# Kernel tuning notes

Measured on AMD Instinct MI355X. Metric: run time of the kernel, lower is better.

Reference implementation:

```python
import jax, jax.numpy as jnp
import numpy as np

N = 50000          # nodes
E = 1_600_000      # edges (avg degree 32)
IN_N, IN_E = 16, 1 # fc_encoder hardwired input dims
H = 128            # per-layer out_node/out_edge channels (out//2 = 64 inner)
BN_EPS = 1e-5


def setup_inputs() -> dict:
    key = jax.random.key(0)
    ks = jax.random.split(key, 32)
    d = {}
    d["x"] = jax.random.normal(ks[0], (N, IN_N), jnp.float32)
    d["edge_attr"] = jax.random.normal(ks[1], (E, IN_E), jnp.float32)
    d["edge_index"] = jax.random.randint(ks[2], (2, E), 0, N)
    i = 3
    for l, (ni, ei) in enumerate([(IN_N, IN_E), (H, H)]):
        s_n = 1.0 / np.sqrt(ni)
        s_e = 1.0 / np.sqrt(ei)
        s_h = 1.0 / np.sqrt(H)
        d[f"l{l}_Wn"] = jax.random.normal(ks[i], (H // 2, ni), jnp.float32) * s_n; i += 1
        d[f"l{l}_We"] = jax.random.normal(ks[i], (H // 2, ei), jnp.float32) * s_e; i += 1
        d[f"l{l}_Wfn"] = jax.random.normal(ks[i], (H, H), jnp.float32) * s_h; i += 1
        d[f"l{l}_bfn"] = jax.random.normal(ks[i], (H,), jnp.float32) * s_h; i += 1
        d[f"l{l}_Wfe"] = jax.random.normal(ks[i], (H, H), jnp.float32) * s_h; i += 1
        d[f"l{l}_bfe"] = jax.random.normal(ks[i], (H,), jnp.float32) * s_h; i += 1
        d[f"l{l}_g"] = jax.random.uniform(ks[i], (H,), jnp.float32, 0.5, 1.5); i += 1
        d[f"l{l}_b"] = jax.random.normal(ks[i], (H,), jnp.float32) * 0.1; i += 1
        d[f"l{l}_rm"] = jax.random.normal(ks[i], (H,), jnp.float32) * 0.1; i += 1
        d[f"l{l}_rv"] = jax.random.uniform(ks[i], (H,), jnp.float32, 0.5, 1.5); i += 1
    return d


def _layer(x, ea, src, dst, Wn, We, Wfn, bfn, Wfe, bfe, g, b, rm, rv):
    # NodeEdgeInteraction_node (eval mode: dropout = identity)
    n1 = jax.nn.relu(x @ Wn.T)            # [N, H/2]
    e1 = jax.nn.relu(ea @ We.T)           # [E, H/2]
    # edge_updater: cat([n1[src] + n1[dst], e1])
    e2 = jnp.concatenate([n1[src] + n1[dst], e1], axis=-1)      # [E, H]
    # propagate: message = e1, sum-aggregate at destination (edge_index[1])
    agg = jax.ops.segment_sum(e1, dst, num_segments=x.shape[0])  # [N, H/2]
    n2 = jnp.concatenate([agg, n1], axis=-1)                     # [N, H]
    n2 = jax.nn.relu(n2 @ Wfn.T + bfn)
    e2 = jax.nn.relu(e2 @ Wfe.T + bfe)
    # BatchNorm1d (eval: running stats)
    n2 = (n2 - rm) * jax.lax.rsqrt(rv + BN_EPS) * g + b
    return n2, e2


def reference(x, edge_attr, edge_index,
              l0_Wn, l0_We, l0_Wfn, l0_bfn, l0_Wfe, l0_bfe, l0_g, l0_b, l0_rm, l0_rv,
              l1_Wn, l1_We, l1_Wfn, l1_bfn, l1_Wfe, l1_bfe, l1_g, l1_b, l1_rm, l1_rv):
    src, dst = edge_index[0], edge_index[1]
    x, edge_attr = _layer(x, edge_attr, src, dst,
                          l0_Wn, l0_We, l0_Wfn, l0_bfn, l0_Wfe, l0_bfe,
                          l0_g, l0_b, l0_rm, l0_rv)
    x, edge_attr = _layer(x, edge_attr, src, dst,
                          l1_Wn, l1_We, l1_Wfn, l1_bfn, l1_Wfe, l1_bfe,
                          l1_g, l1_b, l1_rm, l1_rv)
    return x  # GNNEncoder returns node embeddings only
```

## Files before the change

kernel.cpp:

```cpp
#include <hip/hip_runtime.h>

typedef unsigned short u16;
typedef __attribute__((ext_vector_type(8))) short short8;
typedef __attribute__((ext_vector_type(4))) float floatx4;

#define NN 50000
#define NE 1600000
#define BN_EPS 1e-5f

__device__ __forceinline__ float bfu(u16 u) {
    union { unsigned u32; float f; } v; v.u32 = ((unsigned)u) << 16; return v.f;
}
__device__ __forceinline__ u16 f2bf(float f) {
    union { float f; unsigned u; } v; v.f = f;
    unsigned r = v.u + 0x7FFFu + ((v.u >> 16) & 1u);
    return (u16)(r >> 16);
}
__device__ __forceinline__ float ldf(const void* p, int i, int m) {
    return m ? ((const float*)p)[i] : bfu(((const u16*)p)[i]);
}

__global__ __launch_bounds__(256) void k_detect(const u16* __restrict__ x, int* __restrict__ mode) {
    float mx = 0.f;
    for (int i = threadIdx.x; i < 4096; i += 256) mx = fmaxf(mx, fabsf(bfu(x[i])));
#pragma unroll
    for (int o = 32; o > 0; o >>= 1) mx = fmaxf(mx, __shfl_down(mx, o));
    __shared__ float s[4];
    if ((threadIdx.x & 63) == 0) s[threadIdx.x >> 6] = mx;
    __syncthreads();
    if (threadIdx.x == 0) {
        float m2 = fmaxf(fmaxf(s[0], s[1]), fmaxf(s[2], s[3]));
        mode[0] = (m2 > 1e4f) ? 1 : 0;
    }
}

__global__ __launch_bounds__(256) void k_cvtw(const void* __restrict__ W0, const void* __restrict__ W1,
                                              const void* __restrict__ W2, const void* __restrict__ W3,
                                              const void* __restrict__ W4,
                                              u16* __restrict__ dst, const int* __restrict__ mf) {
    int m = mf[0];
    int i = blockIdx.x * 256 + threadIdx.x;
    const void* src; int off;
    if (i < 16384)      { src = W0; off = i; }
    else if (i < 24576) { src = W1; off = i - 16384; }
    else if (i < 40960) { src = W2; off = i - 24576; }
    else if (i < 49152) { src = W3; off = i - 40960; }
    else                { src = W4; off = i - 49152; }
    dst[i] = m ? f2bf(((const float*)src)[off]) : ((const u16*)src)[off];
}

__global__ __launch_bounds__(256) void k_enc0(const void* __restrict__ x, const void* __restrict__ Wn,
                                              u16* __restrict__ n1, const int* __restrict__ mf) {
    int m = mf[0];
    __shared__ float Wns[64 * 17];
    __shared__ float xsh[4][16];
    int t = threadIdx.x;
    int n0 = blockIdx.x * 4;
    for (int i = t; i < 1024; i += 256) Wns[(i >> 4) * 17 + (i & 15)] = ldf(Wn, i, m);
    if (t < 64) xsh[t >> 4][t & 15] = ldf(x, n0 * 16 + t, m);
    __syncthreads();
    int n = t >> 6, c = t & 63;
    float acc = 0.f;
#pragma unroll
    for (int i = 0; i < 16; i++) acc += xsh[n][i] * Wns[c * 17 + i];
    n1[(n0 + n) * 64 + c] = f2bf(fmaxf(acc, 0.f));
}

__global__ __launch_bounds__(256) void k_esum(const void* __restrict__ ea, const int* __restrict__ ei,
                                              float* __restrict__ sp, float* __restrict__ sn,
                                              const int* __restrict__ mf) {
    int m = mf[0];
    int e = blockIdx.x * 256 + threadIdx.x;
    float a = ldf(ea, e, m);
    int d = ei[NE + e];
    if (a > 0.f) atomicAdd(sp + d, a);
    else if (a < 0.f) atomicAdd(sn + d, a);
}

__global__ void k_pn(const void* __restrict__ We0, const void* __restrict__ Wfe0,
                     float* __restrict__ PN, const int* __restrict__ mf) {
    int m = mf[0];
    int j = threadIdx.x;
    float p = 0.f, n = 0.f;
    for (int k = 0; k < 64; k++) {
        float w = ldf(We0, k, m);
        float wf = ldf(Wfe0, j * 128 + 64 + k, m);
        p += fmaxf(w, 0.f) * wf;
        n += fminf(w, 0.f) * wf;
    }
    PN[j] = p; PN[128 + j] = n;
}

__global__ __launch_bounds__(256) void k_node_l0(
    const u16* __restrict__ n1l0, const float* __restrict__ sp, const float* __restrict__ sn,
    const void* __restrict__ We0, const u16* __restrict__ Wfn0c, const void* __restrict__ bfn0,
    const void* __restrict__ g0, const void* __restrict__ b0,
    const void* __restrict__ rm0, const void* __restrict__ rv0,
    const u16* __restrict__ Wn1c, u16* __restrict__ n1l1, const int* __restrict__ mf) {
    int m = mf[0];
    __shared__ __align__(16) u16 fs[64][136];
    __shared__ __align__(16) u16 xs[64][136];
    int t = threadIdx.x;
    int n0 = blockIdx.x * 64;
    {
        int col = t & 127;
        int rbase = t >> 7;
        float wp = 0.f, wn = 0.f;
        if (col < 64) { float w0 = ldf(We0, col, m); wp = fmaxf(w0, 0.f); wn = fminf(w0, 0.f); }
#pragma unroll
        for (int i = 0; i < 32; i++) {
            int row = rbase + 2 * i;
            int n = n0 + row;
            float v = 0.f;
            if (n < NN) v = (col < 64) ? (wp * sp[n] + wn * sn[n]) : bfu(n1l0[n * 64 + col - 64]);
            fs[row][col] = f2bf(v);
        }
    }
    __syncthreads();
    int lane = t & 63, w = t >> 6, q = lane >> 4, nidx = lane & 15;
    {
        const u16* ar = &fs[w * 16 + nidx][0];
        short8 a0 = *(const short8*)&ar[q * 8];
        short8 a1 = *(const short8*)&ar[32 + q * 8];
        short8 a2 = *(const short8*)&ar[64 + q * 8];
        short8 a3 = *(const short8*)&ar[96 + q * 8];
#pragma unroll
        for (int jt = 0; jt < 8; jt++) {
            int j = jt * 16 + nidx;
            const u16* wr = Wfn0c + j * 128;
            floatx4 acc = {0.f, 0.f, 0.f, 0.f};
            acc = __builtin_amdgcn_mfma_f32_16x16x32_bf16(a0, *(const short8*)&wr[q * 8], acc, 0, 0, 0);
            acc = __builtin_amdgcn_mfma_f32_16x16x32_bf16(a1, *(const short8*)&wr[32 + q * 8], acc, 0, 0, 0);
            acc = __builtin_amdgcn_mfma_f32_16x16x32_bf16(a2, *(const short8*)&wr[64 + q * 8], acc, 0, 0, 0);
            acc = __builtin_amdgcn_mfma_f32_16x16x32_bf16(a3, *(const short8*)&wr[96 + q * 8], acc, 0, 0, 0);
            float bias = ldf(bfn0, j, m);
            float sc = ldf(g0, j, m) * rsqrtf(ldf(rv0, j, m) + BN_EPS);
            float sh = ldf(b0, j, m) - ldf(rm0, j, m) * sc;
#pragma unroll
            for (int r = 0; r < 4; r++) {
                int row = w * 16 + q * 4 + r;
                xs[row][j] = f2bf(fmaxf(acc[r] + bias, 0.f) * sc + sh);
            }
        }
    }
    __syncthreads();
    {
        const u16* ar = &xs[w * 16 + nidx][0];
        short8 a0 = *(const short8*)&ar[q * 8];
        short8 a1 = *(const short8*)&ar[32 + q * 8];
        short8 a2 = *(const short8*)&ar[64 + q * 8];
        short8 a3 = *(const short8*)&ar[96 + q * 8];
#pragma unroll
        for (int jt = 0; jt < 4; jt++) {
            int j = jt * 16 + nidx;
            const u16* wr = Wn1c + j * 128;
            floatx4 acc = {0.f, 0.f, 0.f, 0.f};
            acc = __builtin_amdgcn_mfma_f32_16x16x32_bf16(a0, *(const short8*)&wr[q * 8], acc, 0, 0, 0);
            acc = __builtin_amdgcn_mfma_f32_16x16x32_bf16(a1, *(const short8*)&wr[32 + q * 8], acc, 0, 0, 0);
            acc = __builtin_amdgcn_mfma_f32_16x16x32_bf16(a2, *(const short8*)&wr[64 + q * 8], acc, 0, 0, 0);
            acc = __builtin_amdgcn_mfma_f32_16x16x32_bf16(a3, *(const short8*)&wr[96 + q * 8], acc, 0, 0, 0);
#pragma unroll
            for (int r = 0; r < 4; r++) {
                int row = w * 16 + q * 4 + r;
                int n = n0 + row;
                if (n < NN) n1l1[n * 64 + j] = f2bf(fmaxf(acc[r], 0.f));
            }
        }
    }
}

__global__ __launch_bounds__(256) void k_edge(
    const void* __restrict__ ea, const int* __restrict__ ei,
    const u16* __restrict__ n1l0,
    const u16* __restrict__ Wfe0c, const void* __restrict__ bfe0,
    const float* __restrict__ PN,
    const u16* __restrict__ We1c,
    float* __restrict__ agg, const int* __restrict__ mf) {
    int m = mf[0];
    __shared__ __align__(16) u16 h0s[16][72];
    __shared__ __align__(16) u16 h1s[16][136];
    __shared__ float aes[16];
    __shared__ int dsts[16];
    __shared__ int srcs[16];
    int t = threadIdx.x;
    int e0 = blockIdx.x * 16;
    if (t < 16) {
        int eg = e0 + t;
        aes[t] = ldf(ea, eg, m);
        srcs[t] = ei[eg];
        dsts[t] = ei[NE + eg];
    }
    __syncthreads();
#pragma unroll
    for (int i = 0; i < 4; i++) {
        int idx = t + i * 256;
        int e = idx >> 6, c = idx & 63;
        float v = bfu(n1l0[srcs[e] * 64 + c]) + bfu(n1l0[dsts[e] * 64 + c]);
        h0s[e][c] = f2bf(v);
    }
    __syncthreads();
    int lane = t & 63;
    int w = t >> 6;
    int q = lane >> 4;
    int nidx = lane & 15;
    short8 a0 = *(const short8*)&h0s[nidx][q * 8];
    short8 a1 = *(const short8*)&h0s[nidx][32 + q * 8];
#pragma unroll
    for (int jj = 0; jj < 2; jj++) {
        int jt = 2 * w + jj;
        int j = jt * 16 + nidx;
        const u16* wrow = Wfe0c + j * 128;
        short8 b0 = *(const short8*)&wrow[q * 8];
        short8 b1 = *(const short8*)&wrow[32 + q * 8];
        floatx4 acc = {0.f, 0.f, 0.f, 0.f};
        acc = __builtin_amdgcn_mfma_f32_16x16x32_bf16(a0, b0, acc, 0, 0, 0);
        acc = __builtin_amdgcn_mfma_f32_16x16x32_bf16(a1, b1, acc, 0, 0, 0);
        float bias = ldf(bfe0, j, m);
        float Pj = PN[j], Nj = PN[128 + j];
#pragma unroll
        for (int r = 0; r < 4; r++) {
            int e = q * 4 + r;
            float a = aes[e];
            float v = acc[r] + bias + a * (a > 0.f ? Pj : Nj);
            h1s[e][j] = f2bf(fmaxf(v, 0.f));
        }
    }
    __syncthreads();
    {
        int c = w * 16 + nidx;
        const u16* wrow = We1c + c * 128;
        floatx4 acc = {0.f, 0.f, 0.f, 0.f};
#pragma unroll
        for (int ks = 0; ks < 4; ks++) {
            short8 aa = *(const short8*)&h1s[nidx][ks * 32 + q * 8];
            short8 bb = *(const short8*)&wrow[ks * 32 + q * 8];
            acc = __builtin_amdgcn_mfma_f32_16x16x32_bf16(aa, bb, acc, 0, 0, 0);
        }
#pragma unroll
        for (int r = 0; r < 4; r++) {
            int e = q * 4 + r;
            float v = fmaxf(acc[r], 0.f);
            atomicAdd(agg + dsts[e] * 64 + c, v);
        }
    }
}

__global__ __launch_bounds__(256) void k_node_l1(
    const u16* __restrict__ n1l1, const float* __restrict__ agg,
    const u16* __restrict__ Wfn1c, const void* __restrict__ bfn1,
    const void* __restrict__ g1, const void* __restrict__ b1,
    const void* __restrict__ rm1, const void* __restrict__ rv1,
    void* __restrict__ out, const int* __restrict__ mf) {
    int m = mf[0];
    __shared__ __align__(16) u16 fs[64][136];
    int t = threadIdx.x;
    int n0 = blockIdx.x * 64;
    {
        int col = t & 127;
        int rbase = t >> 7;
#pragma unroll
        for (int i = 0; i < 32; i++) {
            int row = rbase + 2 * i;
            int n = n0 + row;
            float v = 0.f;
            if (n < NN) v = (col < 64) ? agg[n * 64 + col] : bfu(n1l1[n * 64 + col - 64]);
            fs[row][col] = f2bf(v);
        }
    }
    __syncthreads();
    int lane = t & 63, w = t >> 6, q = lane >> 4, nidx = lane & 15;
    const u16* ar = &fs[w * 16 + nidx][0];
    short8 a0 = *(const short8*)&ar[q * 8];
    short8 a1 = *(const short8*)&ar[32 + q * 8];
    short8 a2 = *(const short8*)&ar[64 + q * 8];
    short8 a3 = *(const short8*)&ar[96 + q * 8];
#pragma unroll
    for (int jt = 0; jt < 8; jt++) {
        int j = jt * 16 + nidx;
        const u16* wr = Wfn1c + j * 128;
        floatx4 acc = {0.f, 0.f, 0.f, 0.f};
        acc = __builtin_amdgcn_mfma_f32_16x16x32_bf16(a0, *(const short8*)&wr[q * 8], acc, 0, 0, 0);
        acc = __builtin_amdgcn_mfma_f32_16x16x32_bf16(a1, *(const short8*)&wr[32 + q * 8], acc, 0, 0, 0);
        acc = __builtin_amdgcn_mfma_f32_16x16x32_bf16(a2, *(const short8*)&wr[64 + q * 8], acc, 0, 0, 0);
        acc = __builtin_amdgcn_mfma_f32_16x16x32_bf16(a3, *(const short8*)&wr[96 + q * 8], acc, 0, 0, 0);
        float bias = ldf(bfn1, j, m);
        float sc = ldf(g1, j, m) * rsqrtf(ldf(rv1, j, m) + BN_EPS);
        float sh = ldf(b1, j, m) - ldf(rm1, j, m) * sc;
#pragma unroll
        for (int r = 0; r < 4; r++) {
            int row = w * 16 + q * 4 + r;
            int n = n0 + row;
            if (n < NN) {
                float v = fmaxf(acc[r] + bias, 0.f) * sc + sh;
                if (m) ((float*)out)[n * 128 + j] = v;
                else   ((u16*)out)[n * 128 + j] = f2bf(v);
            }
        }
    }
}

extern "C" void kernel_launch(void* const* d_in, const int* in_sizes, int n_in,
                              void* d_out, int out_size, void* d_ws, size_t ws_size,
                              hipStream_t stream) {
    const void* x    = d_in[0];
    const void* ea   = d_in[1];
    const int*  ei   = (const int*)d_in[2];
    const void* Wn0  = d_in[3];
    const void* We0  = d_in[4];
    const void* Wfn0 = d_in[5];
    const void* bfn0 = d_in[6];
    const void* Wfe0 = d_in[7];
    const void* bfe0 = d_in[8];
    const void* g0   = d_in[9];
    const void* b0   = d_in[10];
    const void* rm0  = d_in[11];
    const void* rv0  = d_in[12];
    const void* Wn1  = d_in[13];
    const void* We1  = d_in[14];
    const void* Wfn1 = d_in[15];
    const void* bfn1 = d_in[16];
    const void* g1   = d_in[19];
    const void* b1   = d_in[20];
    const void* rm1  = d_in[21];
    const void* rv1  = d_in[22];

    float* wsf   = (float*)d_ws;
    float* agg   = wsf;
    u16*   n1l0  = (u16*)(wsf + 3200000);
    u16*   n1l1  = (u16*)(wsf + 4800000);
    float* sp    = wsf + 6400000;
    float* sn    = wsf + 6450000;
    float* PN    = wsf + 6500000;
    u16*   Wc    = (u16*)(wsf + 6500256);
    int*   mode  = (int*)(wsf + 6533024);
    u16* Wfe0c = Wc;
    u16* We1c  = Wc + 16384;
    u16* Wfn0c = Wc + 24576;
    u16* Wn1c  = Wc + 40960;
    u16* Wfn1c = Wc + 49152;

    hipMemsetAsync(sp, 0, 100000 * sizeof(float), stream);
    hipMemsetAsync(agg, 0, 3200000 * sizeof(float), stream);

    k_detect<<<1, 256, 0, stream>>>((const u16*)x, mode);
    k_cvtw<<<256, 256, 0, stream>>>(Wfe0, We1, Wfn0, Wn1, Wfn1, Wc, mode);
    k_enc0<<<12500, 256, 0, stream>>>(x, Wn0, n1l0, mode);
    k_esum<<<6250, 256, 0, stream>>>(ea, ei, sp, sn, mode);
    k_pn<<<1, 128, 0, stream>>>(We0, Wfe0, PN, mode);
    k_node_l0<<<782, 256, 0, stream>>>(n1l0, sp, sn, We0, Wfn0c, bfn0,
                                       g0, b0, rm0, rv0, Wn1c, n1l1, mode);
    k_edge<<<100000, 256, 0, stream>>>(ea, ei, n1l0, Wfe0c, bfe0, PN, We1c, agg, mode);
    k_node_l1<<<782, 256, 0, stream>>>(n1l1, agg, Wfn1c, bfn1,
                                       g1, b1, rm1, rv1, d_out, mode);
}
```

Measured before the change: 709.3 us.

## Sort edges by destination via counting sort and segment-reduce aggregation in edge kernel

Adds a histogram, scan and scatter pass that buckets edges by destination node, packing src and dst into 16-bit halves of one word and storing edge attributes as bf16. The edge kernel then handles 64 edges per block and reduces runs of equal destination in shared memory before issuing atomics, so far fewer atomicAdds hit agg. The separate sp/sn edge-sum kernel is folded into the edge kernel. The cost is extra sort passes with their own atomics and a single-block scan, and the scatter order from atomics is nondeterministic. It also relies on node ids fitting in 16 bits (N=50000) and reuses the n1l1 buffer region for the sorted edge list.

```diff
diff --git a/kernel.cpp b/kernel.cpp
--- a/kernel.cpp
+++ b/kernel.cpp
@@ -66,17 +66,6 @@
     n1[(n0 + n) * 64 + c] = f2bf(fmaxf(acc, 0.f));
 }
 
-__global__ __launch_bounds__(256) void k_esum(const void* __restrict__ ea, const int* __restrict__ ei,
-                                              float* __restrict__ sp, float* __restrict__ sn,
-                                              const int* __restrict__ mf) {
-    int m = mf[0];
-    int e = blockIdx.x * 256 + threadIdx.x;
-    float a = ldf(ea, e, m);
-    int d = ei[NE + e];
-    if (a > 0.f) atomicAdd(sp + d, a);
-    else if (a < 0.f) atomicAdd(sn + d, a);
-}
-
 __global__ void k_pn(const void* __restrict__ We0, const void* __restrict__ Wfe0,
                      float* __restrict__ PN, const int* __restrict__ mf) {
     int m = mf[0];
@@ -89,6 +78,150 @@
         n += fminf(w, 0.f) * wf;
     }
     PN[j] = p; PN[128 + j] = n;
+}
+
+__global__ __launch_bounds__(256) void k_hist(const int* __restrict__ ei, int* __restrict__ off) {
+    int e = blockIdx.x * 256 + threadIdx.x;
+    atomicAdd(off + ei[NE + e], 1);
+}
+
+__global__ __launch_bounds__(1024) void k_scan(int* __restrict__ off) {
+    __shared__ int part[1024];
+    int t = threadIdx.x;
+    int base = t * 49;
+    int lim = 50000 - base; if (lim > 49) lim = 49; if (lim < 0) lim = 0;
+    int s = 0;
+    for (int i = 0; i < lim; i++) s += off[base + i];
+    part[t] = s;
+    __syncthreads();
+    for (int o = 1; o < 1024; o <<= 1) {
+        int v = (t >= o) ? part[t - o] : 0;
+        __syncthreads();
+        part[t] += v;
+        __syncthreads();
+    }
+    int run = (t > 0) ? part[t - 1] : 0;
+    for (int i = 0; i < lim; i++) { int v = off[base + i]; off[base + i] = run; run += v; }
+}
+
+__global__ __launch_bounds__(256) void k_scatter(const int* __restrict__ ei, const void* __restrict__ ea,
+                                                 int* __restrict__ off,
+                                                 unsigned* __restrict__ ssd, u16* __restrict__ sae,
+                                                 const int* __restrict__ mf) {
+    int m = mf[0];
+    int e = blockIdx.x * 256 + threadIdx.x;
+    int srcv = ei[e], d = ei[NE + e];
+    int p = atomicAdd(off + d, 1);
+    ssd[p] = (unsigned)srcv | ((unsigned)d << 16);
+    sae[p] = f2bf(ldf(ea, e, m));
+}
+
+__global__ __launch_bounds__(256) void k_edge(
+    const unsigned* __restrict__ ssd, const u16* __restrict__ sae,
+    const u16* __restrict__ n1l0,
+    const u16* __restrict__ Wfe0c, const void* __restrict__ bfe0,
+    const float* __restrict__ PN,
+    const u16* __restrict__ We1c,
+    float* __restrict__ agg, float* __restrict__ sp, float* __restrict__ sn,
+    const int* __restrict__ mf) {
+    int m = mf[0];
+    __shared__ __align__(16) u16 h0s[64][72];
+    __shared__ __align__(16) u16 h1s[64][136];
+    __shared__ __align__(16) float h2s[64][68];
+    __shared__ float aes[64];
+    __shared__ unsigned sd[64];
+    int t = threadIdx.x;
+    int e0 = blockIdx.x * 64;
+    if (t < 64) {
+        sd[t] = ssd[e0 + t];
+        aes[t] = bfu(sae[e0 + t]);
+    }
+    __syncthreads();
+#pragma unroll
+    for (int i = 0; i < 16; i++) {
+        int idx = i * 256 + t;
+        int e = idx >> 6, c = idx & 63;
+        unsigned p = sd[e];
+        int s = p & 0xFFFF, d = p >> 16;
+        float v = bfu(n1l0[s * 64 + c]) + bfu(n1l0[d * 64 + c]);
+        h0s[e][c] = f2bf(v);
+    }
+    __syncthreads();
+    int lane = t & 63, w = t >> 6, q = lane >> 4, nidx = lane & 15;
+    {
+        const u16* ar = &h0s[w * 16 + nidx][0];
+        short8 a0 = *(const short8*)&ar[q * 8];
+        short8 a1 = *(const short8*)&ar[32 + q * 8];
+#pragma unroll
+        for (int jt = 0; jt < 8; jt++) {
+            int j = jt * 16 + nidx;
+            const u16* wr = Wfe0c + j * 128;
+            floatx4 acc = {0.f, 0.f, 0.f, 0.f};
+            acc = __builtin_amdgcn_mfma_f32_16x16x32_bf16(a0, *(const short8*)&wr[q * 8], acc, 0, 0, 0);
+            acc = __builtin_amdgcn_mfma_f32_16x16x32_bf16(a1, *(const short8*)&wr[32 + q * 8], acc, 0, 0, 0);
+            float bias = ldf(bfe0, j, m);
+            float Pj = PN[j], Nj = PN[128 + j];
+#pragma unroll
+            for (int r = 0; r < 4; r++) {
+                int e = w * 16 + q * 4 + r;
+                float a = aes[e];
+                float v = acc[r] + bias + a * (a > 0.f ? Pj : Nj);
+                h1s[e][j] = f2bf(fmaxf(v, 0.f));
+            }
+        }
+    }
+    __syncthreads();
+    {
+        const u16* ar = &h1s[w * 16 + nidx][0];
+        short8 a0 = *(const short8*)&ar[q * 8];
+        short8 a1 = *(const short8*)&ar[32 + q * 8];
+        short8 a2 = *(const short8*)&ar[64 + q * 8];
+        short8 a3 = *(const short8*)&ar[96 + q * 8];
+#pragma unroll
+        for (int ct = 0; ct < 4; ct++) {
+            int c = ct * 16 + nidx;
+            const u16* wr = We1c + c * 128;
+            floatx4 acc = {0.f, 0.f, 0.f, 0.f};
+            acc = __builtin_amdgcn_mfma_f32_16x16x32_bf16(a0, *(const short8*)&wr[q * 8], acc, 0, 0, 0);
+            acc = __builtin_amdgcn_mfma_f32_16x16x32_bf16(a1, *(const short8*)&wr[32 + q * 8], acc, 0, 0, 0);
+            acc = __builtin_amdgcn_mfma_f32_16x16x32_bf16(a2, *(const short8*)&wr[64 + q * 8], acc, 0, 0, 0);
+            acc = __builtin_amdgcn_mfma_f32_16x16x32_bf16(a3, *(const short8*)&wr[96 + q * 8], acc, 0, 0, 0);
+#pragma unroll
+            for (int r = 0; r < 4; r++) {
+                int e = w * 16 + q * 4 + r;
+                h2s[e][c] = fmaxf(acc[r], 0.f);
+            }
+        }
+    }
+    __syncthreads();
+    if (t < 128) {
+        int c = t & 63;
+        int ebeg = (t >> 6) * 32, eend = ebeg + 32;
+        float s = 0.f;
+        int cur = sd[ebeg] >> 16;
+        for (int e = ebeg; e < eend; e++) {
+            int d = sd[e] >> 16;
+            if (d != cur) { atomicAdd(agg + cur * 64 + c, s); s = 0.f; cur = d; }
+            s += h2s[e][c];
+        }
+        atomicAdd(agg + cur * 64 + c, s);
+    } else if (t < 130) {
+        int ebeg = (t - 128) * 32, eend = ebeg + 32;
+        float p = 0.f, n = 0.f;
+        int cur = sd[ebeg] >> 16;
+        for (int e = ebeg; e < eend; e++) {
+            int d = sd[e] >> 16;
+            if (d != cur) {
+                if (p != 0.f) atomicAdd(sp + cur, p);
+                if (n != 0.f) atomicAdd(sn + cur, n);
+                p = 0.f; n = 0.f; cur = d;
+            }
+            float a = aes[e];
+            p += fmaxf(a, 0.f); n += fminf(a, 0.f);
+        }
+        if (p != 0.f) atomicAdd(sp + cur, p);
+        if (n != 0.f) atomicAdd(sn + cur, n);
+    }
 }
 
 __global__ __launch_bounds__(256) void k_node_l0(
@@ -165,82 +298,6 @@
                 int n = n0 + row;
                 if (n < NN) n1l1[n * 64 + j] = f2bf(fmaxf(acc[r], 0.f));
             }
-        }
-    }
-}
-
-__global__ __launch_bounds__(256) void k_edge(
-    const void* __restrict__ ea, const int* __restrict__ ei,
-    const u16* __restrict__ n1l0,
-    const u16* __restrict__ Wfe0c, const void* __restrict__ bfe0,
-    const float* __restrict__ PN,
-    const u16* __restrict__ We1c,
-    float* __restrict__ agg, const int* __restrict__ mf) {
-    int m = mf[0];
-    __shared__ __align__(16) u16 h0s[16][72];
-    __shared__ __align__(16) u16 h1s[16][136];
-    __shared__ float aes[16];
-    __shared__ int dsts[16];
-    __shared__ int srcs[16];
-    int t = threadIdx.x;
-    int e0 = blockIdx.x * 16;
-    if (t < 16) {
-        int eg = e0 + t;
-        aes[t] = ldf(ea, eg, m);
-        srcs[t] = ei[eg];
-        dsts[t] = ei[NE + eg];
-    }
-    __syncthreads();
-#pragma unroll
-    for (int i = 0; i < 4; i++) {
-        int idx = t + i * 256;
-        int e = idx >> 6, c = idx & 63;
-        float v = bfu(n1l0[srcs[e] * 64 + c]) + bfu(n1l0[dsts[e] * 64 + c]);
-        h0s[e][c] = f2bf(v);
-    }
-    __syncthreads();
-    int lane = t & 63;
-    int w = t >> 6;
-    int q = lane >> 4;
-    int nidx = lane & 15;
-    short8 a0 = *(const short8*)&h0s[nidx][q * 8];
-    short8 a1 = *(const short8*)&h0s[nidx][32 + q * 8];
-#pragma unroll
-    for (int jj = 0; jj < 2; jj++) {
-        int jt = 2 * w + jj;
-        int j = jt * 16 + nidx;
-        const u16* wrow = Wfe0c + j * 128;
-        short8 b0 = *(const short8*)&wrow[q * 8];
-        short8 b1 = *(const short8*)&wrow[32 + q * 8];
-        floatx4 acc = {0.f, 0.f, 0.f, 0.f};
-        acc = __builtin_amdgcn_mfma_f32_16x16x32_bf16(a0, b0, acc, 0, 0, 0);
-        acc = __builtin_amdgcn_mfma_f32_16x16x32_bf16(a1, b1, acc, 0, 0, 0);
-        float bias = ldf(bfe0, j, m);
-        float Pj = PN[j], Nj = PN[128 + j];
-#pragma unroll
-        for (int r = 0; r < 4; r++) {
-            int e = q * 4 + r;
-            float a = aes[e];
-            float v = acc[r] + bias + a * (a > 0.f ? Pj : Nj);
-            h1s[e][j] = f2bf(fmaxf(v, 0.f));
-        }
-    }
-    __syncthreads();
-    {
-        int c = w * 16 + nidx;
-        const u16* wrow = We1c + c * 128;
-        floatx4 acc = {0.f, 0.f, 0.f, 0.f};
-#pragma unroll
-        for (int ks = 0; ks < 4; ks++) {
-            short8 aa = *(const short8*)&h1s[nidx][ks * 32 + q * 8];
-            short8 bb = *(const short8*)&wrow[ks * 32 + q * 8];
-            acc = __builtin_amdgcn_mfma_f32_16x16x32_bf16(aa, bb, acc, 0, 0, 0);
-        }
-#pragma unroll
-        for (int r = 0; r < 4; r++) {
-            int e = q * 4 + r;
-            float v = fmaxf(acc[r], 0.f);
-            atomicAdd(agg + dsts[e] * 64 + c, v);
         }
     }
 }
@@ -324,15 +381,18 @@
     const void* rm1  = d_in[21];
     const void* rv1  = d_in[22];
 
-    float* wsf   = (float*)d_ws;
-    float* agg   = wsf;
-    u16*   n1l0  = (u16*)(wsf + 3200000);
-    u16*   n1l1  = (u16*)(wsf + 4800000);
-    float* sp    = wsf + 6400000;
-    float* sn    = wsf + 6450000;
-    float* PN    = wsf + 6500000;
-    u16*   Wc    = (u16*)(wsf + 6500256);
-    int*   mode  = (int*)(wsf + 6533024);
+    float* wsf = (float*)d_ws;
+    float*    agg  = wsf;
+    u16*      n1l0 = (u16*)(wsf + 3200000);
+    unsigned* ssd  = (unsigned*)(wsf + 4800000);
+    u16*      n1l1 = (u16*)(wsf + 4800000);
+    u16*      sae  = (u16*)(wsf + 6400000);
+    float*    sp   = wsf + 7200000;
+    float*    sn   = wsf + 7250000;
+    float*    PN   = wsf + 7300000;
+    u16*      Wc   = (u16*)(wsf + 7300256);
+    int*      off  = (int*)(wsf + 7333024);
+    int*      mode = (int*)(wsf + 7383024);
     u16* Wfe0c = Wc;
     u16* We1c  = Wc + 16384;
     u16* Wfn0c = Wc + 24576;
@@ -341,15 +401,19 @@
 
     hipMemsetAsync(sp, 0, 100000 * sizeof(float), stream);
     hipMemsetAsync(agg, 0, 3200000 * sizeof(float), stream);
+    hipMemsetAsync(off, 0, 50000 * sizeof(int), stream);
 
     k_detect<<<1, 256, 0, stream>>>((const u16*)x, mode);
     k_cvtw<<<256, 256, 0, stream>>>(Wfe0, We1, Wfn0, Wn1, Wfn1, Wc, mode);
     k_enc0<<<12500, 256, 0, stream>>>(x, Wn0, n1l0, mode);
-    k_esum<<<6250, 256, 0, stream>>>(ea, ei, sp, sn, mode);
     k_pn<<<1, 128, 0, stream>>>(We0, Wfe0, PN, mode);
+    k_hist<<<6250, 256, 0, stream>>>(ei, off);
+    k_scan<<<1, 1024, 0, stream>>>(off);
+    k_scatter<<<6250, 256, 0, stream>>>(ei, ea, off, ssd, sae, mode);
+    k_edge<<<25000, 256, 0, stream>>>(ssd, sae, n1l0, Wfe0c, bfe0, PN, We1c,
+                                      agg, sp, sn, mode);
     k_node_l0<<<782, 256, 0, stream>>>(n1l0, sp, sn, We0, Wfn0c, bfn0,
                                        g0, b0, rm0, rv0, Wn1c, n1l1, mode);
-    k_edge<<<100000, 256, 0, stream>>>(ea, ei, n1l0, Wfe0c, bfe0, PN, We1c, agg, mode);
     k_node_l1<<<782, 256, 0, stream>>>(n1l1, agg, Wfn1c, bfn1,
                                        g1, b1, rm1, rv1, d_out, mode);
 }
```

Result: slower. 899.6 us (+26.8%).
